# Performance work log

Hardware: AMD Instinct MI355X
Metric: run time of the kernel (lower is better)

## Reference

```python
import jax, jax.numpy as jnp
import numpy as np

COMMITMENT_COST = 0.25


def setup_inputs() -> dict:
    key = jax.random.key(0)
    k1, k2 = jax.random.split(key)
    inputs = jax.random.normal(k1, (32, 64, 64, 64), dtype=jnp.float32)  # BCHW, C=embedding_dim
    codebook = jax.random.normal(k2, (1024, 64), dtype=jnp.float32)      # [n_embeddings, embedding_dim]
    return {"inputs": inputs, "codebook": codebook}


def reference(inputs, codebook):
    B, C, H, W = inputs.shape
    K, D = codebook.shape  # D == C
    x = jnp.transpose(inputs, (0, 2, 3, 1))          # BHWC
    flat = x.reshape(-1, D)                          # [N, D]
    # squared-euclidean distances [N, K]
    distances = (jnp.sum(flat * flat, axis=1, keepdims=True)
                 + jnp.sum(codebook * codebook, axis=1)
                 - 2.0 * flat @ codebook.T)
    logits = -distances
    idx = jnp.argmax(logits, axis=-1)                # [N]
    oh = jax.nn.one_hot(idx, K, dtype=flat.dtype)    # [N, K]
    # straight-through one-hot
    oh_st = oh + logits - jax.lax.stop_gradient(logits)
    oh_encodings = jnp.transpose(oh_st.reshape(B, H * W, K), (0, 2, 1))  # b d n
    # quantized computed under no_grad in torch -> full stop_gradient
    quantized = jax.lax.stop_gradient(oh_st @ codebook).reshape(x.shape)  # BHWC
    e_latent_loss = jnp.mean((quantized - x) ** 2)
    loss = COMMITMENT_COST * e_latent_loss
    q_st = x + jax.lax.stop_gradient(quantized - x)  # straight-through output
    avg_probs = jnp.mean(oh_st, axis=0)              # [K]
    perplexity = jnp.exp(-jnp.sum(avg_probs * jnp.log(avg_probs + 1e-10)))
    return (loss, jnp.transpose(q_st, (0, 3, 1, 2)), perplexity, oh_encodings)
```

## Files before the change

kernel.cpp:

```cpp
#include <hip/hip_runtime.h>
#include <math.h>

typedef _Float16 half8 __attribute__((ext_vector_type(8)));
typedef float f32x4 __attribute__((ext_vector_type(4)));

#define NBLK     1024
#define Q_OFF    1
#define PERP_OFF 8388609
#define OH_OFF   8388610
#define LOSS_N   8388608.0f

#define CB2_OFF_B 16384

__global__ __launch_bounds__(256) void k0_prep(const float* __restrict__ cb,
                                               float* __restrict__ cnorm,
                                               int* __restrict__ hist,
                                               char* __restrict__ cb2) {
  int k = blockIdx.x * 256 + threadIdx.x;
  hist[k] = 0;
  const float* row = cb + (size_t)k * 64;
  const float4* r4 = (const float4*)row;
  float s = 0.f;
#pragma unroll
  for (int i = 0; i < 16; ++i) {
    float4 v = r4[i];
    s += v.x * v.x + v.y * v.y + v.z * v.z + v.w * v.w;
  }
  cnorm[k] = s;

  int chunk = k >> 7, c = k & 127;
  int xv = (c & 7) << 4;
  char* base = cb2 + chunk * 32768 + c * 128;
#pragma unroll
  for (int d16 = 0; d16 < 8; ++d16) {
    half8 hh, ll;
#pragma unroll
    for (int i = 0; i < 8; ++i) {
      float v = row[d16 * 8 + i];
      _Float16 h = (_Float16)v;
      hh[i] = h;
      ll[i] = (_Float16)(v - (float)h);
    }
    int off = (d16 * 16) ^ xv;
    *(half8*)(base + off) = hh;
    *(half8*)(base + 16384 + off) = ll;
  }
}

__global__ __launch_bounds__(256, 4) void k1_main(
    const float* __restrict__ in, const float* __restrict__ cb,
    const uint4* __restrict__ cb2, const float* __restrict__ cnorm,
    int* __restrict__ hist, float* __restrict__ partial,
    float* __restrict__ out) {
  __shared__ uint4 lds_cb[2048];
  __shared__ int bestk_s[128];
  __shared__ float red[256];

  const int tid = threadIdx.x;
  const int bid = blockIdx.x;
  const int w = tid >> 6, l = tid & 63, q = l & 15, g = l >> 4;
  const int b = bid >> 5;
  const int hw0 = (bid & 31) << 7;

  half8 ah[2][2], al[2][2];
  {
    const float* xb = in + ((size_t)b << 18);
#pragma unroll
    for (int a = 0; a < 2; ++a) {
      const int hw = hw0 + w * 32 + a * 16 + q;
#pragma unroll
      for (int ks = 0; ks < 2; ++ks) {
#pragma unroll
        for (int i = 0; i < 8; ++i) {
          float v = xb[((size_t)(ks * 32 + g * 8 + i) << 12) + hw];
          _Float16 h = (_Float16)v;
          ah[a][ks][i] = h;
          al[a][ks][i] = (_Float16)(v - (float)h);
        }
      }
    }
  }

  float bd0[4], bd1[4];
  int bk0[4], bk1[4];
#pragma unroll
  for (int j = 0; j < 4; ++j) { bd0[j] = bd1[j] = 3.4e38f; bk0[j] = bk1[j] = 0; }

  const int xorv = (q & 7) << 4;
  const int offh0 = q * 128 + ((g * 16) ^ xorv);
  const int offh1 = q * 128 + ((64 + g * 16) ^ xorv);
  float* ohrow0 = out + OH_OFF + ((size_t)b << 22) + hw0;
  const float2 z2 = make_float2(0.f, 0.f);

  for (int ch = 0; ch < 8; ++ch) {
    __syncthreads();
    const uint4* src = cb2 + (size_t)ch * 2048;
#pragma unroll
    for (int i = 0; i < 8; ++i) lds_cb[i * 256 + tid] = src[i * 256 + tid];
    __syncthreads();

    const char* base = (const char*)lds_cb;
    const int cbase = ch << 7;
#pragma unroll
    for (int tb = 0; tb < 8; ++tb) {
      {
        const int row = cbase + w * 32 + tb * 4;
#pragma unroll
        for (int r = 0; r < 4; ++r)
          ((float2*)(ohrow0 + (size_t)(row + r) * 4096))[l] = z2;
      }
      const char* tbase = base + tb * 2048;
      half8 bh0 = *(const half8*)(tbase + offh0);
      half8 bh1 = *(const half8*)(tbase + offh1);
      half8 bl0 = *(const half8*)(tbase + 16384 + offh0);
      half8 bl1 = *(const half8*)(tbase + 16384 + offh1);
      const int code = cbase + tb * 16 + q;
      const float cn = cnorm[code];
      const f32x4 z = {0.f, 0.f, 0.f, 0.f};
      f32x4 s = __builtin_amdgcn_mfma_f32_16x16x32_f16(ah[0][0], bh0, z, 0, 0, 0);
      s = __builtin_amdgcn_mfma_f32_16x16x32_f16(al[0][0], bh0, s, 0, 0, 0);
      s = __builtin_amdgcn_mfma_f32_16x16x32_f16(ah[0][0], bl0, s, 0, 0, 0);
      f32x4 t = __builtin_amdgcn_mfma_f32_16x16x32_f16(ah[0][1], bh1, z, 0, 0, 0);
      t = __builtin_amdgcn_mfma_f32_16x16x32_f16(al[0][1], bh1, t, 0, 0, 0);
      t = __builtin_amdgcn_mfma_f32_16x16x32_f16(ah[0][1], bl1, t, 0, 0, 0);
      s = s + t;
#pragma unroll
      for (int j = 0; j < 4; ++j) {
        float d = fmaf(-2.f, s[j], cn);
        if (d < bd0[j]) { bd0[j] = d; bk0[j] = code; }
      }
      f32x4 u = __builtin_amdgcn_mfma_f32_16x16x32_f16(ah[1][0], bh0, z, 0, 0, 0);
      u = __builtin_amdgcn_mfma_f32_16x16x32_f16(al[1][0], bh0, u, 0, 0, 0);
      u = __builtin_amdgcn_mfma_f32_16x16x32_f16(ah[1][0], bl0, u, 0, 0, 0);
      f32x4 v = __builtin_amdgcn_mfma_f32_16x16x32_f16(ah[1][1], bh1, z, 0, 0, 0);
      v = __builtin_amdgcn_mfma_f32_16x16x32_f16(al[1][1], bh1, v, 0, 0, 0);
      v = __builtin_amdgcn_mfma_f32_16x16x32_f16(ah[1][1], bl1, v, 0, 0, 0);
      u = u + v;
#pragma unroll
      for (int j = 0; j < 4; ++j) {
        float d = fmaf(-2.f, u[j], cn);
        if (d < bd1[j]) { bd1[j] = d; bk1[j] = code; }
      }
    }
  }

#pragma unroll
  for (int m = 1; m < 16; m <<= 1) {
#pragma unroll
    for (int j = 0; j < 4; ++j) {
      float od = __shfl_xor(bd0[j], m, 64);
      int ok = __shfl_xor(bk0[j], m, 64);
      if (od < bd0[j] || (od == bd0[j] && ok < bk0[j])) { bd0[j] = od; bk0[j] = ok; }
      od = __shfl_xor(bd1[j], m, 64);
      ok = __shfl_xor(bk1[j], m, 64);
      if (od < bd1[j] || (od == bd1[j] && ok < bk1[j])) { bd1[j] = od; bk1[j] = ok; }
    }
  }
  if (q == 0) {
#pragma unroll
    for (int j = 0; j < 4; ++j) {
      bestk_s[w * 32 + g * 4 + j] = bk0[j];
      bestk_s[w * 32 + 16 + g * 4 + j] = bk1[j];
    }
  }
  __syncthreads();

  const int p = tid & 127, hf = tid >> 7;
  const int kq = bestk_s[p];
  if (hf == 0) {
    out[OH_OFF + ((size_t)b << 22) + ((size_t)kq << 12) + hw0 + p] = 1.0f;
    atomicAdd(&hist[kq], 1);
  }
  float lsum = 0.f;
  {
    const float* xb = in + ((size_t)b << 18) + hw0 + p;
    float* yb = out + Q_OFF + ((size_t)b << 18) + hw0 + p;
    const float* qrow = cb + (size_t)kq * 64;
#pragma unroll
    for (int c = 0; c < 32; ++c) {
      const int cc = hf * 32 + c;
      float x = xb[(size_t)cc << 12];
      float f = qrow[cc] - x;
      lsum += f * f;
      yb[(size_t)cc << 12] = x + f;
    }
  }
  red[tid] = lsum;
  __syncthreads();
#pragma unroll
  for (int sft = 128; sft > 0; sft >>= 1) {
    if (tid < sft) red[tid] += red[tid + sft];
    __syncthreads();
  }
  if (tid == 0) partial[bid] = red[0];
}

__global__ __launch_bounds__(1024) void k2_finalize(const int* __restrict__ hist,
                                                    const float* __restrict__ partial,
                                                    float* __restrict__ out) {
  __shared__ float red[1024];
  int tid = threadIdx.x;

  red[tid] = partial[tid];
  __syncthreads();
  for (int s = 512; s > 0; s >>= 1) {
    if (tid < s) red[tid] += red[tid + s];
    __syncthreads();
  }
  if (tid == 0) out[0] = 0.25f * (red[0] / LOSS_N);
  __syncthreads();

  float pr = (float)hist[tid] * (1.0f / 131072.0f);
  red[tid] = pr * logf(pr + 1e-10f);
  __syncthreads();
  for (int s = 512; s > 0; s >>= 1) {
    if (tid < s) red[tid] += red[tid + s];
    __syncthreads();
  }
  if (tid == 0) out[PERP_OFF] = expf(-red[0]);
}

extern "C" void kernel_launch(void* const* d_in, const int* in_sizes, int n_in,
                              void* d_out, int out_size, void* d_ws, size_t ws_size,
                              hipStream_t stream) {
  const float* in = (const float*)d_in[0];
  const float* cb = (const float*)d_in[1];
  float* out = (float*)d_out;

  float* cnorm   = (float*)d_ws;
  int*   hist    = (int*)d_ws + 1024;
  float* partial = (float*)d_ws + 2048;
  char*  cb2b    = (char*)d_ws + CB2_OFF_B;

  k0_prep<<<4, 256, 0, stream>>>(cb, cnorm, hist, cb2b);
  k1_main<<<NBLK, 256, 0, stream>>>(in, cb, (const uint4*)cb2b, cnorm, hist,
                                    partial, out);
  k2_finalize<<<1, 1024, 0, stream>>>(hist, partial, out);
}
```

Measured before the change: 268.6 us.

## Stream one-hot zeros contiguously with nontemporal stores, scatter ones in separate kernel

```diff
diff --git a/kernel.cpp b/kernel.cpp
--- a/kernel.cpp
+++ b/kernel.cpp
@@ -3,6 +3,7 @@
 
 typedef _Float16 half8 __attribute__((ext_vector_type(8)));
 typedef float f32x4 __attribute__((ext_vector_type(4)));
+typedef float f32x2 __attribute__((ext_vector_type(2)));
 
 #define NBLK     1024
 #define Q_OFF    1
@@ -11,6 +12,7 @@
 #define LOSS_N   8388608.0f
 
 #define CB2_OFF_B 16384
+#define IDX_OFF_W 69632
 
 __global__ __launch_bounds__(256) void k0_prep(const float* __restrict__ cb,
                                                float* __restrict__ cnorm,
@@ -28,9 +30,8 @@
   }
   cnorm[k] = s;
 
-  int chunk = k >> 7, c = k & 127;
-  int xv = (c & 7) << 4;
-  char* base = cb2 + chunk * 32768 + c * 128;
+  int tile = k >> 4, c = k & 15;
+  char* base = cb2 + tile * 4096;
 #pragma unroll
   for (int d16 = 0; d16 < 8; ++d16) {
     half8 hh, ll;
@@ -41,18 +42,17 @@
       hh[i] = h;
       ll[i] = (_Float16)(v - (float)h);
     }
-    int off = (d16 * 16) ^ xv;
+    int off = (d16 >> 2) * 1024 + c * 64 + (d16 & 3) * 16;
     *(half8*)(base + off) = hh;
-    *(half8*)(base + 16384 + off) = ll;
+    *(half8*)(base + 2048 + off) = ll;
   }
 }
 
 __global__ __launch_bounds__(256, 4) void k1_main(
     const float* __restrict__ in, const float* __restrict__ cb,
-    const uint4* __restrict__ cb2, const float* __restrict__ cnorm,
+    const char* __restrict__ cb2, const float* __restrict__ cnorm,
     int* __restrict__ hist, float* __restrict__ partial,
-    float* __restrict__ out) {
-  __shared__ uint4 lds_cb[2048];
+    int* __restrict__ idx, float* __restrict__ out) {
   __shared__ int bestk_s[128];
   __shared__ float red[256];
 
@@ -86,61 +86,49 @@
 #pragma unroll
   for (int j = 0; j < 4; ++j) { bd0[j] = bd1[j] = 3.4e38f; bk0[j] = bk1[j] = 0; }
 
-  const int xorv = (q & 7) << 4;
-  const int offh0 = q * 128 + ((g * 16) ^ xorv);
-  const int offh1 = q * 128 + ((64 + g * 16) ^ xorv);
-  float* ohrow0 = out + OH_OFF + ((size_t)b << 22) + hw0;
-  const float2 z2 = make_float2(0.f, 0.f);
-
-  for (int ch = 0; ch < 8; ++ch) {
-    __syncthreads();
-    const uint4* src = cb2 + (size_t)ch * 2048;
-#pragma unroll
-    for (int i = 0; i < 8; ++i) lds_cb[i * 256 + tid] = src[i * 256 + tid];
-    __syncthreads();
-
-    const char* base = (const char*)lds_cb;
-    const int cbase = ch << 7;
-#pragma unroll
-    for (int tb = 0; tb < 8; ++tb) {
-      {
-        const int row = cbase + w * 32 + tb * 4;
-#pragma unroll
-        for (int r = 0; r < 4; ++r)
-          ((float2*)(ohrow0 + (size_t)(row + r) * 4096))[l] = z2;
-      }
-      const char* tbase = base + tb * 2048;
-      half8 bh0 = *(const half8*)(tbase + offh0);
-      half8 bh1 = *(const half8*)(tbase + offh1);
-      half8 bl0 = *(const half8*)(tbase + 16384 + offh0);
-      half8 bl1 = *(const half8*)(tbase + 16384 + offh1);
-      const int code = cbase + tb * 16 + q;
-      const float cn = cnorm[code];
-      const f32x4 z = {0.f, 0.f, 0.f, 0.f};
-      f32x4 s = __builtin_amdgcn_mfma_f32_16x16x32_f16(ah[0][0], bh0, z, 0, 0, 0);
-      s = __builtin_amdgcn_mfma_f32_16x16x32_f16(al[0][0], bh0, s, 0, 0, 0);
-      s = __builtin_amdgcn_mfma_f32_16x16x32_f16(ah[0][0], bl0, s, 0, 0, 0);
-      f32x4 t = __builtin_amdgcn_mfma_f32_16x16x32_f16(ah[0][1], bh1, z, 0, 0, 0);
-      t = __builtin_amdgcn_mfma_f32_16x16x32_f16(al[0][1], bh1, t, 0, 0, 0);
-      t = __builtin_amdgcn_mfma_f32_16x16x32_f16(ah[0][1], bl1, t, 0, 0, 0);
-      s = s + t;
-#pragma unroll
-      for (int j = 0; j < 4; ++j) {
-        float d = fmaf(-2.f, s[j], cn);
-        if (d < bd0[j]) { bd0[j] = d; bk0[j] = code; }
-      }
-      f32x4 u = __builtin_amdgcn_mfma_f32_16x16x32_f16(ah[1][0], bh0, z, 0, 0, 0);
-      u = __builtin_amdgcn_mfma_f32_16x16x32_f16(al[1][0], bh0, u, 0, 0, 0);
-      u = __builtin_amdgcn_mfma_f32_16x16x32_f16(ah[1][0], bl0, u, 0, 0, 0);
-      f32x4 v = __builtin_amdgcn_mfma_f32_16x16x32_f16(ah[1][1], bh1, z, 0, 0, 0);
-      v = __builtin_amdgcn_mfma_f32_16x16x32_f16(al[1][1], bh1, v, 0, 0, 0);
-      v = __builtin_amdgcn_mfma_f32_16x16x32_f16(ah[1][1], bl1, v, 0, 0, 0);
-      u = u + v;
-#pragma unroll
-      for (int j = 0; j < 4; ++j) {
-        float d = fmaf(-2.f, u[j], cn);
-        if (d < bd1[j]) { bd1[j] = d; bk1[j] = code; }
-      }
+  const int boff = q * 64 + g * 16;
+  f32x2* ohz = (f32x2*)(out + OH_OFF);
+  const f32x2 z2 = {0.f, 0.f};
+  const size_t slab = (size_t)bid * 65536 + tid;
+
+  for (int tb = 0; tb < 64; ++tb) {
+    const char* tbase = cb2 + tb * 4096 + boff;
+    half8 bh0 = *(const half8*)(tbase);
+    half8 bh1 = *(const half8*)(tbase + 1024);
+    half8 bl0 = *(const half8*)(tbase + 2048);
+    half8 bl1 = *(const half8*)(tbase + 3072);
+    const int code = tb * 16 + q;
+    const float cn = cnorm[code];
+    const f32x4 z = {0.f, 0.f, 0.f, 0.f};
+    f32x4 s = __builtin_amdgcn_mfma_f32_16x16x32_f16(ah[0][0], bh0, z, 0, 0, 0);
+    s = __builtin_amdgcn_mfma_f32_16x16x32_f16(al[0][0], bh0, s, 0, 0, 0);
+    s = __builtin_amdgcn_mfma_f32_16x16x32_f16(ah[0][0], bl0, s, 0, 0, 0);
+    f32x4 t = __builtin_amdgcn_mfma_f32_16x16x32_f16(ah[0][1], bh1, z, 0, 0, 0);
+    t = __builtin_amdgcn_mfma_f32_16x16x32_f16(al[0][1], bh1, t, 0, 0, 0);
+    t = __builtin_amdgcn_mfma_f32_16x16x32_f16(ah[0][1], bl1, t, 0, 0, 0);
+    s = s + t;
+#pragma unroll
+    for (int j = 0; j < 4; ++j) {
+      float d = fmaf(-2.f, s[j], cn);
+      if (d < bd0[j]) { bd0[j] = d; bk0[j] = code; }
+    }
+    f32x4 u = __builtin_amdgcn_mfma_f32_16x16x32_f16(ah[1][0], bh0, z, 0, 0, 0);
+    u = __builtin_amdgcn_mfma_f32_16x16x32_f16(al[1][0], bh0, u, 0, 0, 0);
+    u = __builtin_amdgcn_mfma_f32_16x16x32_f16(ah[1][0], bl0, u, 0, 0, 0);
+    f32x4 v = __builtin_amdgcn_mfma_f32_16x16x32_f16(ah[1][1], bh1, z, 0, 0, 0);
+    v = __builtin_amdgcn_mfma_f32_16x16x32_f16(al[1][1], bh1, v, 0, 0, 0);
+    v = __builtin_amdgcn_mfma_f32_16x16x32_f16(ah[1][1], bl1, v, 0, 0, 0);
+    u = u + v;
+#pragma unroll
+    for (int j = 0; j < 4; ++j) {
+      float d = fmaf(-2.f, u[j], cn);
+      if (d < bd1[j]) { bd1[j] = d; bk1[j] = code; }
+    }
+    {
+      size_t zb = slab + (size_t)tb * 1024;
+#pragma unroll
+      for (int r = 0; r < 4; ++r)
+        __builtin_nontemporal_store(z2, &ohz[zb + r * 256]);
     }
   }
 
@@ -168,7 +156,7 @@
   const int p = tid & 127, hf = tid >> 7;
   const int kq = bestk_s[p];
   if (hf == 0) {
-    out[OH_OFF + ((size_t)b << 22) + ((size_t)kq << 12) + hw0 + p] = 1.0f;
+    idx[bid * 128 + p] = kq;
     atomicAdd(&hist[kq], 1);
   }
   float lsum = 0.f;
@@ -220,6 +208,15 @@
   if (tid == 0) out[PERP_OFF] = expf(-red[0]);
 }
 
+__global__ __launch_bounds__(256) void k3_scatter(const int* __restrict__ idx,
+                                                  float* __restrict__ out) {
+  int n = blockIdx.x * 256 + threadIdx.x;
+  int k = idx[n];
+  int b = n >> 12;
+  int pos = n & 4095;
+  out[OH_OFF + ((((size_t)b << 10) + (size_t)k) << 12) + pos] = 1.0f;
+}
+
 extern "C" void kernel_launch(void* const* d_in, const int* in_sizes, int n_in,
                               void* d_out, int out_size, void* d_ws, size_t ws_size,
                               hipStream_t stream) {
@@ -231,9 +228,10 @@
   int*   hist    = (int*)d_ws + 1024;
   float* partial = (float*)d_ws + 2048;
   char*  cb2b    = (char*)d_ws + CB2_OFF_B;
+  int*   idx     = (int*)d_ws + IDX_OFF_W;
 
   k0_prep<<<4, 256, 0, stream>>>(cb, cnorm, hist, cb2b);
-  k1_main<<<NBLK, 256, 0, stream>>>(in, cb, (const uint4*)cb2b, cnorm, hist,
-                                    partial, out);
+  k1_main<<<NBLK, 256, 0, stream>>>(in, cb, cb2b, cnorm, hist, partial, idx, out);
   k2_finalize<<<1, 1024, 0, stream>>>(hist, partial, out);
-}
+  k3_scatter<<<512, 256, 0, stream>>>(idx, out);
+}
```

After: 224.9 us. -16.2%, faster.
